# Kernel tuning notes

Hardware: AMD Instinct MI355X
Metric: run time of the kernel (lower is better)

Reference implementation:

```python
import jax, jax.numpy as jnp
import numpy as np

N = 50000
E = 800000
NODE_IN = 128
HID = 256
OUT = 256
EDGE_DIM = 16
HEADS = 4
CH = HID // HEADS  # 64
NEG_SLOPE = 0.2


def _init_linear(key, fan_in, fan_out):
    k1, k2 = jax.random.split(key)
    bound = 1.0 / np.sqrt(fan_in)
    W = jax.random.uniform(k1, (fan_in, fan_out), jnp.float32, -bound, bound)
    b = jax.random.uniform(k2, (fan_out,), jnp.float32, -bound, bound)
    return W, b


def setup_inputs() -> dict:
    key = jax.random.key(0)
    ks = jax.random.split(key, 12)
    node_feats = jax.random.normal(ks[0], (N, NODE_IN), jnp.float32)
    edge_index = jax.random.randint(ks[1], (2, E), 0, N, jnp.int64)
    edge_attr = jax.random.normal(ks[2], (E, EDGE_DIM), jnp.float32)

    Wnp, bnp = _init_linear(ks[3], NODE_IN, HID)           # node_proj
    Wep, bep = _init_linear(ks[4], EDGE_DIM, HID)          # edge_proj
    # GATConv 1: in = 2*HID, out per head = CH
    Wg1, _ = _init_linear(ks[5], 2 * HID, HEADS * CH)
    as1 = jax.random.normal(ks[6], (HEADS, CH), jnp.float32) * 0.1
    ad1 = jax.random.normal(ks[7], (HEADS, CH), jnp.float32) * 0.1
    bg1 = jnp.zeros((HEADS * CH,), jnp.float32)
    # GATConv 2: in = HID, out per head = OUT//HEADS
    Wg2, _ = _init_linear(ks[8], HID, HEADS * (OUT // HEADS))
    as2 = jax.random.normal(ks[9], (HEADS, OUT // HEADS), jnp.float32) * 0.1
    ad2 = jax.random.normal(ks[10], (HEADS, OUT // HEADS), jnp.float32) * 0.1
    bg2 = jnp.zeros((OUT,), jnp.float32)
    Wo, bo = _init_linear(ks[11], OUT, OUT)                # out_proj
    return {
        "node_feats": node_feats, "edge_attr": edge_attr,
        "Wnp": Wnp, "bnp": bnp, "Wep": Wep, "bep": bep,
        "Wg1": Wg1, "as1": as1, "ad1": ad1, "bg1": bg1,
        "Wg2": Wg2, "as2": as2, "ad2": ad2, "bg2": bg2,
        "Wo": Wo, "bo": bo,
        "edge_index": edge_index,
    }


def scatter_mean(src, index, num_nodes):
    # mean of edge features grouped by target node; empty groups -> 0 (count clamped to 1)
    s = jax.ops.segment_sum(src, index, num_segments=num_nodes)
    cnt = jax.ops.segment_sum(jnp.ones((src.shape[0],), src.dtype), index, num_segments=num_nodes)
    return s / jnp.maximum(cnt, 1.0)[:, None]


def gat_conv(x, src, dst, W, att_src, att_dst, bias, num_nodes, heads, ch):
    # PyG GATConv with add_self_loops=True (loops appended by caller via src/dst),
    # concat=True, negative_slope=0.2.
    xh = (x @ W).reshape(num_nodes, heads, ch)             # [N,H,C]
    a_src = jnp.sum(xh * att_src, axis=-1)                 # [N,H]
    a_dst = jnp.sum(xh * att_dst, axis=-1)                 # [N,H]
    logits = jax.nn.leaky_relu(a_src[src] + a_dst[dst], NEG_SLOPE)  # [E,H]
    # segment softmax over incoming edges of each destination node
    m = jax.ops.segment_max(logits, dst, num_segments=num_nodes)    # [N,H]
    ex = jnp.exp(logits - m[dst])
    denom = jax.ops.segment_sum(ex, dst, num_segments=num_nodes)    # [N,H]
    alpha = ex / denom[dst]                                          # [E,H]
    msg = xh[src] * alpha[:, :, None]                                # [E,H,C]
    out = jax.ops.segment_sum(msg, dst, num_segments=num_nodes)      # [N,H,C]
    return out.reshape(num_nodes, heads * ch) + bias


def reference(node_feats, edge_attr, Wnp, bnp, Wep, bep,
              Wg1, as1, ad1, bg1, Wg2, as2, ad2, bg2, Wo, bo, edge_index):
    n = node_feats.shape[0]
    x = node_feats @ Wnp + bnp                                       # [N,HID]
    # EdgeAggregator: mean of edge_attr over target nodes, then edge_proj
    nef = scatter_mean(edge_attr, edge_index[1], n)                  # [N,EDGE_DIM]
    nef = nef @ Wep + bep                                            # [N,HID]
    x = jnp.concatenate([x, nef], axis=-1)                           # [N,2*HID]
    # add self loops once (same augmented edge set for both GAT layers)
    loops = jnp.arange(n, dtype=edge_index.dtype)
    src = jnp.concatenate([edge_index[0], loops])
    dst = jnp.concatenate([edge_index[1], loops])
    x = jax.nn.elu(gat_conv(x, src, dst, Wg1, as1, ad1, bg1, n, HEADS, CH))
    # dropout is identity in eval mode
    x = jax.nn.elu(gat_conv(x, src, dst, Wg2, as2, ad2, bg2, n, HEADS, OUT // HEADS))
    return x @ Wo + bo
```

## Files before the change

kernel.cpp:

```cpp
#include <hip/hip_runtime.h>
#include <hip/hip_bf16.h>


#define HEADS 4

typedef __attribute__((ext_vector_type(8))) short bf16x8;
typedef __attribute__((ext_vector_type(4))) float f32x4;
typedef __attribute__((ext_vector_type(4))) unsigned short u16x4;

__device__ __forceinline__ unsigned short f2b(float v) {
    __hip_bfloat16 b = __float2bfloat16(v);
    return __builtin_bit_cast(unsigned short, b);
}
__device__ __forceinline__ float b2f(unsigned short u) {
    __hip_bfloat16 b = __builtin_bit_cast(__hip_bfloat16, u);
    return __bfloat162float(b);
}
__device__ __forceinline__ void split_hilo(float v, unsigned short& h, unsigned short& l) {
    h = f2b(v);
    l = f2b(v - b2f(h));
}
__device__ __forceinline__ unsigned short f2h(float v) {
    _Float16 h = (_Float16)v;
    return __builtin_bit_cast(unsigned short, h);
}
__device__ __forceinline__ float h2f(unsigned short u) {
    return (float)__builtin_bit_cast(_Float16, u);
}
__device__ __forceinline__ void gl2lds16(const unsigned short* g, unsigned short* l) {
    __builtin_amdgcn_global_load_lds(
        (const __attribute__((address_space(1))) unsigned int*)g,
        (__attribute__((address_space(3))) unsigned int*)l,
        16, 0, 0);
}


__global__ __launch_bounds__(256) void count_kernel(
    const int* __restrict__ dst, int* __restrict__ cnt, int E)
{
    int e = blockIdx.x * 256 + threadIdx.x;
    if (e < E) atomicAdd(&cnt[dst[e]], 1);
}

__global__ __launch_bounds__(256) void scan1_kernel(
    const int* __restrict__ cnt, int* __restrict__ chunk_sum, int N)
{
    __shared__ int sd[256];
    int t = threadIdx.x;
    int n = blockIdx.x * 256 + t;
    sd[t] = (n < N) ? (cnt[n] + 1) : 0;
    __syncthreads();
    for (int o = 128; o > 0; o >>= 1) {
        if (t < o) sd[t] += sd[t + o];
        __syncthreads();
    }
    if (t == 0) chunk_sum[blockIdx.x] = sd[0];
}

__global__ __launch_bounds__(256) void scan2_kernel(
    const int* __restrict__ chunk_sum, int* __restrict__ chunk_off, int nchunk)
{
    __shared__ int sd[256];
    __shared__ int carry;
    int t = threadIdx.x;
    if (t == 0) carry = 0;
    __syncthreads();
    for (int b = 0; b < nchunk; b += 256) {
        int i = b + t;
        int v = (i < nchunk) ? chunk_sum[i] : 0;
        sd[t] = v;
        __syncthreads();
        for (int o = 1; o < 256; o <<= 1) {
            int x = (t >= o) ? sd[t - o] : 0;
            __syncthreads();
            sd[t] += x;
            __syncthreads();
        }
        if (i < nchunk) chunk_off[i] = carry + sd[t] - v;
        __syncthreads();
        if (t == 0) carry += sd[255];
        __syncthreads();
    }
}

__global__ __launch_bounds__(256) void scan3_kernel(
    const int* __restrict__ cnt, const int* __restrict__ chunk_off,
    int* __restrict__ rowptr, int* __restrict__ fillptr,
    int* __restrict__ col, int* __restrict__ eid, int N)
{
    __shared__ int sd[256];
    int t = threadIdx.x;
    int n = blockIdx.x * 256 + t;
    int v = (n < N) ? (cnt[n] + 1) : 0;
    sd[t] = v;
    __syncthreads();
    for (int o = 1; o < 256; o <<= 1) {
        int x = (t >= o) ? sd[t - o] : 0;
        __syncthreads();
        sd[t] += x;
        __syncthreads();
    }
    if (n < N) {
        int incl = sd[t];
        int r = chunk_off[blockIdx.x] + incl - v;
        rowptr[n] = r;
        col[r] = n;
        eid[r] = -1;
        fillptr[n] = r + 1;
        if (n == N - 1) rowptr[N] = chunk_off[blockIdx.x] + incl;
    }
}

__global__ __launch_bounds__(256) void fill_kernel(
    const int* __restrict__ src, const int* __restrict__ dst,
    int* __restrict__ fillptr, int* __restrict__ col, int* __restrict__ eid, int E)
{
    int e = blockIdx.x * 256 + threadIdx.x;
    if (e >= E) return;
    int d = dst[e];
    int p = atomicAdd(&fillptr[d], 1);
    col[p] = src[e];
    eid[p] = e;
}

__global__ __launch_bounds__(256) void nef_csr_kernel(
    const float* __restrict__ ea, const int* __restrict__ rowptr,
    const int* __restrict__ eid,
    unsigned short* __restrict__ AH, unsigned short* __restrict__ AL, int N)
{
    int n = blockIdx.x * 4 + (threadIdx.x >> 6);
    if (n >= N) return;
    int t = threadIdx.x & 63;
    int f = t & 15, g = t >> 4;
    int base = rowptr[n], end = rowptr[n + 1];
    int deg = end - base - 1;
    float acc = 0.0f;
    for (int j = base + 1 + g; j < end; j += 4) {
        int e = eid[j];
        acc += ea[(size_t)e * 16 + f];
    }
    acc += __shfl_down(acc, 32, 64);
    acc += __shfl_down(acc, 16, 64);
    if (t < 16) {
        float v = acc / fmaxf((float)deg, 1.0f);
        unsigned short h, l;
        split_hilo(v, h, l);
        AH[(size_t)n * 160 + 128 + t] = h;
        AL[(size_t)n * 160 + 128 + t] = l;
    } else if (t < 32) {
        AH[(size_t)n * 160 + 128 + t] = 0;
        AL[(size_t)n * 160 + 128 + t] = 0;
    }
}

__global__ __launch_bounds__(256) void conv_hilo_strided_kernel(
    const float* __restrict__ X,
    unsigned short* __restrict__ H, unsigned short* __restrict__ L, int total)
{
    int base = (blockIdx.x * 256 + threadIdx.x) * 2;
    if (base >= total) return;
    #pragma unroll
    for (int i = 0; i < 2; i++) {
        int e = base + i;
        int row = e >> 7, c = e & 127;
        unsigned short h, l;
        split_hilo(X[e], h, l);
        H[(size_t)row * 160 + c] = h;
        L[(size_t)row * 160 + c] = l;
    }
}

__global__ __launch_bounds__(256) void compose_w1_kernel(
    const float* __restrict__ Wnp, const float* __restrict__ Wep,
    const float* __restrict__ bnp, const float* __restrict__ bep,
    const float* __restrict__ Wg1,
    float* __restrict__ Wc, float* __restrict__ c1)
{
    int idx = blockIdx.x * 256 + threadIdx.x;
    if (idx >= 145 * 256) return;
    int i = idx >> 8, j = idx & 255;
    float s = 0.0f;
    if (i < 128) {
        for (int k = 0; k < 256; k++) s += Wnp[i * 256 + k] * Wg1[(size_t)k * 256 + j];
        Wc[i * 256 + j] = s;
    } else if (i < 144) {
        int ii = i - 128;
        for (int k = 0; k < 256; k++) s += Wep[ii * 256 + k] * Wg1[(size_t)(256 + k) * 256 + j];
        Wc[i * 256 + j] = s;
    } else {
        for (int k = 0; k < 256; k++)
            s += bnp[k] * Wg1[(size_t)k * 256 + j] + bep[k] * Wg1[(size_t)(256 + k) * 256 + j];
        c1[j] = s;
    }
}

__device__ __forceinline__ void pack_one(
    const float* __restrict__ W, int K, int KP, int idx,
    unsigned short* __restrict__ Ph, unsigned short* __restrict__ Pl)
{
    int tile = idx >> 9, w = idx & 511, lane = w >> 3, j = w & 7;
    int nk = KP >> 5;
    int ctile = tile / nk, t = tile % nk;
    int k = t * 32 + ((lane >> 4) << 3) + j;
    int n = (ctile << 4) + (lane & 15);
    float v = (k < K) ? W[(size_t)k * 256 + n] : 0.0f;
    unsigned short h, l;
    split_hilo(v, h, l);
    Ph[idx] = h;
    Pl[idx] = l;
}

__global__ __launch_bounds__(256) void pack3_w_kernel(
    const float* __restrict__ Wc,  unsigned short* __restrict__ PcH,  unsigned short* __restrict__ PcL,
    const float* __restrict__ Wg2, unsigned short* __restrict__ Pg2H, unsigned short* __restrict__ Pg2L,
    const float* __restrict__ Wo,  unsigned short* __restrict__ PoH,  unsigned short* __restrict__ PoL)
{
    const int S0 = 160 * 256;
    const int S1 = S0 + 256 * 256;
    const int S2 = S1 + 256 * 256;
    int idx = blockIdx.x * 256 + threadIdx.x;
    if (idx < S0) {
        pack_one(Wc, 144, 160, idx, PcH, PcL);
    } else if (idx < S1) {
        pack_one(Wg2, 256, 256, idx - S0, Pg2H, Pg2L);
    } else if (idx < S2) {
        pack_one(Wo, 256, 256, idx - S1, PoH, PoL);
    }
}

template <int KSTEPS, int OMODE, bool FUSE_ATT>
__global__ __launch_bounds__(256, 5) void mfma_gemm_kernel(
    const unsigned short* __restrict__ Ah, const unsigned short* __restrict__ Al,
    int lda,
    const unsigned short* __restrict__ Ph, const unsigned short* __restrict__ Pl,
    const float* __restrict__ bias,
    float* __restrict__ Cf,
    unsigned short* __restrict__ Ch, unsigned short* __restrict__ Cl,
    int ldc, int col_off, int Nrows,
    const float* __restrict__ att_src, const float* __restrict__ att_dst,
    float* __restrict__ a_srcO, float* __restrict__ a_dstO)
{
    __shared__ unsigned short ldsB[2][2][8][512];
    int tid = threadIdx.x;
    int wave = tid >> 6, lane = tid & 63;
    int quad = lane >> 4, m16 = lane & 15;
    int rowblk = blockIdx.x, colhalf = blockIdx.y;
    int ctile0 = colhalf * 8;

    int row = rowblk * 64 + wave * 16 + m16;
    bool rowok = row < Nrows;
    const unsigned short* arh = Ah + (size_t)row * lda;
    const unsigned short* arl = Al + (size_t)row * lda;

    auto stage = [&](int t, int buf) {
        #pragma unroll
        for (int q = 0; q < 2; q++) {
            int c = wave * 2 + q;
            size_t gb = ((size_t)((ctile0 + c) * KSTEPS + t)) * 512 + lane * 8;
            gl2lds16(Ph + gb, &ldsB[buf][0][c][0]);
            gl2lds16(Pl + gb, &ldsB[buf][1][c][0]);
        }
    };
    auto loadA = [&](int t, bf16x8& h, bf16x8& l) {
        int k = t * 32 + quad * 8;
        h = (bf16x8){};
        l = (bf16x8){};
        if (rowok) {
            h = *(const bf16x8*)(arh + k);
            l = *(const bf16x8*)(arl + k);
        }
    };

    f32x4 acc[8] = {};
    bf16x8 ah2[2], al2[2];
    loadA(0, ah2[0], al2[0]);
    stage(0, 0);
    __syncthreads();

    #pragma unroll
    for (int t = 0; t < KSTEPS; t++) {
        const int buf = t & 1;
        if (t + 1 < KSTEPS) {
            stage(t + 1, buf ^ 1);
            loadA(t + 1, ah2[(t + 1) & 1], al2[(t + 1) & 1]);
        }
        #pragma unroll
        for (int c = 0; c < 8; c++) {
            bf16x8 b_h = *(const bf16x8*)&ldsB[buf][0][c][lane * 8];
            bf16x8 b_l = *(const bf16x8*)&ldsB[buf][1][c][lane * 8];
            acc[c] = __builtin_amdgcn_mfma_f32_16x16x32_bf16(ah2[buf], b_h, acc[c], 0, 0, 0);
            acc[c] = __builtin_amdgcn_mfma_f32_16x16x32_bf16(al2[buf], b_h, acc[c], 0, 0, 0);
            acc[c] = __builtin_amdgcn_mfma_f32_16x16x32_bf16(ah2[buf], b_l, acc[c], 0, 0, 0);
        }
        if (t + 1 < KSTEPS) __syncthreads();
    }

    #pragma unroll
    for (int c = 0; c < 8; c++) {
        int ocol = (ctile0 + c) * 16 + m16;
        float bv = bias ? bias[ocol] : 0.0f;
        #pragma unroll
        for (int r = 0; r < 4; r++) {
            int orow = rowblk * 64 + wave * 16 + quad * 4 + r;
            if (orow >= Nrows) continue;
            float v = acc[c][r] + bv;
            size_t oidx = (size_t)orow * ldc + col_off + ocol;
            if (OMODE == 1) {
                unsigned short h, l;
                split_hilo(v, h, l);
                Ch[oidx] = h;
                Cl[oidx] = l;
            } else if (OMODE == 2) {
                Ch[oidx] = f2h(v);
            } else {
                Cf[oidx] = v;
            }
        }
    }

    if (FUSE_ATT) {
        float ps[4][2] = {}, pd[4][2] = {};
        #pragma unroll
        for (int c = 0; c < 8; c++) {
            int ocol = (ctile0 + c) * 16 + m16;
            float bv = bias ? bias[ocol] : 0.0f;
            float asv = att_src[ocol];
            float adv = att_dst[ocol];
            int hl = c >> 2;
            #pragma unroll
            for (int r = 0; r < 4; r++) {
                float v = acc[c][r] + bv;
                ps[r][hl] += v * asv;
                pd[r][hl] += v * adv;
            }
        }
        #pragma unroll
        for (int r = 0; r < 4; r++) {
            #pragma unroll
            for (int hl = 0; hl < 2; hl++) {
                float s = ps[r][hl], d = pd[r][hl];
                #pragma unroll
                for (int o = 8; o > 0; o >>= 1) {
                    s += __shfl_down(s, o, 64);
                    d += __shfl_down(d, o, 64);
                }
                if (m16 == 0) {
                    int orow = rowblk * 64 + wave * 16 + quad * 4 + r;
                    if (orow < Nrows) {
                        int gh = colhalf * 2 + hl;
                        a_srcO[orow * 4 + gh] = s;
                        a_dstO[orow * 4 + gh] = d;
                    }
                }
            }
        }
    }
}

__global__ __launch_bounds__(256) void edge_w_kernel(
    const int* __restrict__ rowptr, const int* __restrict__ col,
    const float* __restrict__ a_src, const float* __restrict__ a_dst,
    float* __restrict__ wq, float* __restrict__ den, int N)
{
    int n = blockIdx.x * 4 + (threadIdx.x >> 6);
    if (n >= N) return;
    int lane = threadIdx.x & 63;
    int base = rowptr[n], end = rowptr[n + 1];
    float4 ad = *(const float4*)&a_dst[n * 4];
    float4 ds = {0.0f, 0.0f, 0.0f, 0.0f};
    for (int j = base + lane; j < end; j += 64) {
        int s = col[j];
        float4 as4 = *(const float4*)&a_src[s * 4];
        float l0 = as4.x + ad.x, l1 = as4.y + ad.y;
        float l2 = as4.z + ad.z, l3 = as4.w + ad.w;
        l0 = fmaxf(l0, 0.2f * l0);
        l1 = fmaxf(l1, 0.2f * l1);
        l2 = fmaxf(l2, 0.2f * l2);
        l3 = fmaxf(l3, 0.2f * l3);
        float4 wv = {__expf(l0), __expf(l1), __expf(l2), __expf(l3)};
        *(float4*)&wq[(size_t)j * 4] = wv;
        ds.x += wv.x; ds.y += wv.y; ds.z += wv.z; ds.w += wv.w;
    }
    #pragma unroll
    for (int o = 32; o > 0; o >>= 1) {
        ds.x += __shfl_down(ds.x, o, 64);
        ds.y += __shfl_down(ds.y, o, 64);
        ds.z += __shfl_down(ds.z, o, 64);
        ds.w += __shfl_down(ds.w, o, 64);
    }
    if (lane == 0) *(float4*)&den[n * 4] = ds;
}

__global__ __launch_bounds__(256) void gat_agg_csr_kernel(
    const unsigned short* __restrict__ xh,
    const int* __restrict__ rowptr, const int* __restrict__ col,
    const float* __restrict__ wq, const float* __restrict__ den,
    const float* __restrict__ bias,
    unsigned short* __restrict__ outH, unsigned short* __restrict__ outL, int N)
{
    int t = threadIdx.x;
    int n = blockIdx.x * 4 + (t >> 6);
    if (n >= N) return;
    int c = t & 63;
    int h = c >> 4;
    int base = rowptr[n], end = rowptr[n + 1];
    int e1 = end - 1;
    float inv = 1.0f / den[n * 4 + h];
    const unsigned short* xcol = xh + (c << 2);

    float4 acc = {0.0f, 0.0f, 0.0f, 0.0f};
    for (int j = base; j < end; j += 4) {
        int j1 = j + 1 < e1 ? j + 1 : e1;
        int j2 = j + 2 < e1 ? j + 2 : e1;
        int j3 = j + 3 < e1 ? j + 3 : e1;
        int s0 = col[j], s1 = col[j1], s2 = col[j2], s3 = col[j3];
        float w0 = wq[(size_t)j * 4 + h];
        float w1 = (j + 1 < end) ? wq[(size_t)j1 * 4 + h] : 0.0f;
        float w2 = (j + 2 < end) ? wq[(size_t)j2 * 4 + h] : 0.0f;
        float w3 = (j + 3 < end) ? wq[(size_t)j3 * 4 + h] : 0.0f;
        u16x4 x0 = *(const u16x4*)(xcol + (size_t)s0 * 256);
        u16x4 x1 = *(const u16x4*)(xcol + (size_t)s1 * 256);
        u16x4 x2 = *(const u16x4*)(xcol + (size_t)s2 * 256);
        u16x4 x3 = *(const u16x4*)(xcol + (size_t)s3 * 256);
        acc.x += w0 * h2f(x0[0]) + w1 * h2f(x1[0]) + w2 * h2f(x2[0]) + w3 * h2f(x3[0]);
        acc.y += w0 * h2f(x0[1]) + w1 * h2f(x1[1]) + w2 * h2f(x2[1]) + w3 * h2f(x3[1]);
        acc.z += w0 * h2f(x0[2]) + w1 * h2f(x1[2]) + w2 * h2f(x2[2]) + w3 * h2f(x3[2]);
        acc.w += w0 * h2f(x0[3]) + w1 * h2f(x1[3]) + w2 * h2f(x2[3]) + w3 * h2f(x3[3]);
    }

    float4 bv = *(const float4*)(bias + (c << 2));
    float o0 = acc.x * inv + bv.x;
    float o1 = acc.y * inv + bv.y;
    float o2 = acc.z * inv + bv.z;
    float o3 = acc.w * inv + bv.w;
    o0 = (o0 > 0.0f) ? o0 : (__expf(o0) - 1.0f);
    o1 = (o1 > 0.0f) ? o1 : (__expf(o1) - 1.0f);
    o2 = (o2 > 0.0f) ? o2 : (__expf(o2) - 1.0f);
    o3 = (o3 > 0.0f) ? o3 : (__expf(o3) - 1.0f);
    u16x4 H, L;
    split_hilo(o0, ((unsigned short*)&H)[0], ((unsigned short*)&L)[0]);
    split_hilo(o1, ((unsigned short*)&H)[1], ((unsigned short*)&L)[1]);
    split_hilo(o2, ((unsigned short*)&H)[2], ((unsigned short*)&L)[2]);
    split_hilo(o3, ((unsigned short*)&H)[3], ((unsigned short*)&L)[3]);
    *(u16x4*)(&outH[(size_t)n * 256 + (c << 2)]) = H;
    *(u16x4*)(&outL[(size_t)n * 256 + (c << 2)]) = L;
}


extern "C" void kernel_launch(void* const* d_in, const int* in_sizes, int n_in,
                              void* d_out, int out_size, void* d_ws, size_t ws_size,
                              hipStream_t stream)
{
    const float* node_feats = (const float*)d_in[0];
    const float* edge_attr  = (const float*)d_in[1];
    const float* Wnp = (const float*)d_in[2];
    const float* bnp = (const float*)d_in[3];
    const float* Wep = (const float*)d_in[4];
    const float* bep = (const float*)d_in[5];
    const float* Wg1 = (const float*)d_in[6];
    const float* as1 = (const float*)d_in[7];
    const float* ad1 = (const float*)d_in[8];
    const float* bg1 = (const float*)d_in[9];
    const float* Wg2 = (const float*)d_in[10];
    const float* as2 = (const float*)d_in[11];
    const float* ad2 = (const float*)d_in[12];
    const float* bg2 = (const float*)d_in[13];
    const float* Wo  = (const float*)d_in[14];
    const float* bo  = (const float*)d_in[15];
    const int*   ei  = (const int*)d_in[16];

    const int N = in_sizes[0] / 128;
    const int E = in_sizes[16] / 2;
    const int* src = ei;
    const int* dst = ei + E;
    const int nchunk = (N + 255) / 256;
    const int EN = E + N;

    typedef unsigned short u16;

    char* base = (char*)d_ws;
    size_t off = 0;
    auto alloc = [&](size_t bytes) -> char* {
        char* p = base + off;
        off += (bytes + 255) & ~(size_t)255;
        return p;
    };
    u16* xhh = (u16*)alloc((size_t)N * 256 * 2);
    u16* R2  = (u16*)alloc((size_t)N * 512 * 2);
    u16* R3  = (u16*)alloc((size_t)N * 512 * 2);
    float* a_src = (float*)alloc((size_t)N * 4 * 4);
    float* a_dst = (float*)alloc((size_t)N * 4 * 4);
    float* wq    = (float*)alloc((size_t)EN * 4 * 4);
    float* den   = (float*)alloc((size_t)N * 4 * 4);
    float* Wc    = (float*)alloc(144 * 256 * 4);
    float* c1    = (float*)alloc(256 * 4);
    u16* PcH  = (u16*)alloc(160 * 256 * 2);
    u16* PcL  = (u16*)alloc(160 * 256 * 2);
    u16* Pg2H = (u16*)alloc(256 * 256 * 2);
    u16* Pg2L = (u16*)alloc(256 * 256 * 2);
    u16* PoH  = (u16*)alloc(256 * 256 * 2);
    u16* PoL  = (u16*)alloc(256 * 256 * 2);
    int* cnt       = (int*)alloc((size_t)N * 4);
    int* rowptr    = (int*)alloc((size_t)(N + 1) * 4);
    int* fillptr   = (int*)alloc((size_t)N * 4);
    int* chunk_sum = (int*)alloc((size_t)nchunk * 4);
    int* chunk_off = (int*)alloc((size_t)nchunk * 4);
    int* colv      = (int*)alloc((size_t)EN * 4);
    int* eid       = (int*)alloc((size_t)EN * 4);

    u16* AcatH = R2;
    u16* AcatL = R3;
    u16* x3H = R2;
    u16* x3L = R2 + (size_t)N * 256;
    u16* x4H = R3;
    u16* x4L = R3 + (size_t)N * 256;

    float* out = (float*)d_out;
    dim3 ggrid((N + 63) / 64, 2);

    hipMemsetAsync(cnt, 0, (size_t)N * sizeof(int), stream);
    count_kernel<<<(E + 255) / 256, 256, 0, stream>>>(dst, cnt, E);
    scan1_kernel<<<nchunk, 256, 0, stream>>>(cnt, chunk_sum, N);
    scan2_kernel<<<1, 256, 0, stream>>>(chunk_sum, chunk_off, nchunk);
    scan3_kernel<<<nchunk, 256, 0, stream>>>(cnt, chunk_off, rowptr, fillptr, colv, eid, N);
    fill_kernel<<<(E + 255) / 256, 256, 0, stream>>>(src, dst, fillptr, colv, eid, E);

    nef_csr_kernel<<<(N + 3) / 4, 256, 0, stream>>>(edge_attr, rowptr, eid, AcatH, AcatL, N);
    conv_hilo_strided_kernel<<<((N * 128) / 2 + 255) / 256, 256, 0, stream>>>(
        node_feats, AcatH, AcatL, N * 128);
    compose_w1_kernel<<<145, 256, 0, stream>>>(Wnp, Wep, bnp, bep, Wg1, Wc, c1);
    {
        const int total = 160 * 256 + 256 * 256 + 256 * 256;
        pack3_w_kernel<<<(total + 255) / 256, 256, 0, stream>>>(
            Wc, PcH, PcL, Wg2, Pg2H, Pg2L, Wo, PoH, PoL);
    }

    mfma_gemm_kernel<5, 2, true><<<ggrid, 256, 0, stream>>>(
        AcatH, AcatL, 160, PcH, PcL, c1, nullptr, xhh, nullptr, 256, 0, N,
        as1, ad1, a_src, a_dst);
    edge_w_kernel<<<(N + 3) / 4, 256, 0, stream>>>(
        rowptr, colv, a_src, a_dst, wq, den, N);
    gat_agg_csr_kernel<<<(N + 3) / 4, 256, 0, stream>>>(
        xhh, rowptr, colv, wq, den, bg1, x3H, x3L, N);

    mfma_gemm_kernel<8, 2, true><<<ggrid, 256, 0, stream>>>(
        x3H, x3L, 256, Pg2H, Pg2L, nullptr, nullptr, xhh, nullptr, 256, 0, N,
        as2, ad2, a_src, a_dst);
    edge_w_kernel<<<(N + 3) / 4, 256, 0, stream>>>(
        rowptr, colv, a_src, a_dst, wq, den, N);
    gat_agg_csr_kernel<<<(N + 3) / 4, 256, 0, stream>>>(
        xhh, rowptr, colv, wq, den, bg2, x4H, x4L, N);

    mfma_gemm_kernel<8, 0, false><<<ggrid, 256, 0, stream>>>(
        x4H, x4L, 256, PoH, PoL, bo, out, nullptr, nullptr, 256, 0, N,
        nullptr, nullptr, nullptr, nullptr);
}
```

Before: 571.5 us.

## Fuse edge softmax weights into aggregation and store GEMM inputs as fp16

```diff
diff --git a/kernel.cpp b/kernel.cpp
--- a/kernel.cpp
+++ b/kernel.cpp
@@ -7,6 +7,7 @@
 typedef __attribute__((ext_vector_type(8))) short bf16x8;
 typedef __attribute__((ext_vector_type(4))) float f32x4;
 typedef __attribute__((ext_vector_type(4))) unsigned short u16x4;
+typedef __attribute__((ext_vector_type(8))) unsigned short u16x8;
 
 __device__ __forceinline__ unsigned short f2b(float v) {
     __hip_bfloat16 b = __float2bfloat16(v);
@@ -126,7 +127,7 @@
 __global__ __launch_bounds__(256) void nef_csr_kernel(
     const float* __restrict__ ea, const int* __restrict__ rowptr,
     const int* __restrict__ eid,
-    unsigned short* __restrict__ AH, unsigned short* __restrict__ AL, int N)
+    unsigned short* __restrict__ AF, int N)
 {
     int n = blockIdx.x * 4 + (threadIdx.x >> 6);
     if (n >= N) return;
@@ -143,19 +144,14 @@
     acc += __shfl_down(acc, 16, 64);
     if (t < 16) {
         float v = acc / fmaxf((float)deg, 1.0f);
-        unsigned short h, l;
-        split_hilo(v, h, l);
-        AH[(size_t)n * 160 + 128 + t] = h;
-        AL[(size_t)n * 160 + 128 + t] = l;
+        AF[(size_t)n * 160 + 128 + t] = f2h(v);
     } else if (t < 32) {
-        AH[(size_t)n * 160 + 128 + t] = 0;
-        AL[(size_t)n * 160 + 128 + t] = 0;
-    }
-}
-
-__global__ __launch_bounds__(256) void conv_hilo_strided_kernel(
-    const float* __restrict__ X,
-    unsigned short* __restrict__ H, unsigned short* __restrict__ L, int total)
+        AF[(size_t)n * 160 + 128 + t] = 0;
+    }
+}
+
+__global__ __launch_bounds__(256) void conv_f16_strided_kernel(
+    const float* __restrict__ X, unsigned short* __restrict__ AF, int total)
 {
     int base = (blockIdx.x * 256 + threadIdx.x) * 2;
     if (base >= total) return;
@@ -163,10 +159,7 @@
     for (int i = 0; i < 2; i++) {
         int e = base + i;
         int row = e >> 7, c = e & 127;
-        unsigned short h, l;
-        split_hilo(X[e], h, l);
-        H[(size_t)row * 160 + c] = h;
-        L[(size_t)row * 160 + c] = l;
+        AF[(size_t)row * 160 + c] = f2h(X[e]);
     }
 }
 
@@ -228,7 +221,7 @@
     }
 }
 
-template <int KSTEPS, int OMODE, bool FUSE_ATT>
+template <int KSTEPS, int AMODE, int OMODE, bool FUSE_ATT>
 __global__ __launch_bounds__(256, 5) void mfma_gemm_kernel(
     const unsigned short* __restrict__ Ah, const unsigned short* __restrict__ Al,
     int lda,
@@ -250,7 +243,7 @@
     int row = rowblk * 64 + wave * 16 + m16;
     bool rowok = row < Nrows;
     const unsigned short* arh = Ah + (size_t)row * lda;
-    const unsigned short* arl = Al + (size_t)row * lda;
+    const unsigned short* arl = (AMODE == 0) ? (Al + (size_t)row * lda) : nullptr;
 
     auto stage = [&](int t, int buf) {
         #pragma unroll
@@ -266,8 +259,20 @@
         h = (bf16x8){};
         l = (bf16x8){};
         if (rowok) {
-            h = *(const bf16x8*)(arh + k);
-            l = *(const bf16x8*)(arl + k);
+            if (AMODE == 0) {
+                h = *(const bf16x8*)(arh + k);
+                l = *(const bf16x8*)(arl + k);
+            } else {
+                u16x8 v = *(const u16x8*)(arh + k);
+                #pragma unroll
+                for (int i = 0; i < 8; i++) {
+                    float f = h2f(v[i]);
+                    unsigned short hh, ll;
+                    split_hilo(f, hh, ll);
+                    ((unsigned short*)&h)[i] = hh;
+                    ((unsigned short*)&l)[i] = ll;
+                }
+            }
         }
     };
 
@@ -357,77 +362,108 @@
     }
 }
 
-__global__ __launch_bounds__(256) void edge_w_kernel(
-    const int* __restrict__ rowptr, const int* __restrict__ col,
-    const float* __restrict__ a_src, const float* __restrict__ a_dst,
-    float* __restrict__ wq, float* __restrict__ den, int N)
-{
-    int n = blockIdx.x * 4 + (threadIdx.x >> 6);
-    if (n >= N) return;
-    int lane = threadIdx.x & 63;
-    int base = rowptr[n], end = rowptr[n + 1];
-    float4 ad = *(const float4*)&a_dst[n * 4];
-    float4 ds = {0.0f, 0.0f, 0.0f, 0.0f};
-    for (int j = base + lane; j < end; j += 64) {
-        int s = col[j];
-        float4 as4 = *(const float4*)&a_src[s * 4];
-        float l0 = as4.x + ad.x, l1 = as4.y + ad.y;
-        float l2 = as4.z + ad.z, l3 = as4.w + ad.w;
-        l0 = fmaxf(l0, 0.2f * l0);
-        l1 = fmaxf(l1, 0.2f * l1);
-        l2 = fmaxf(l2, 0.2f * l2);
-        l3 = fmaxf(l3, 0.2f * l3);
-        float4 wv = {__expf(l0), __expf(l1), __expf(l2), __expf(l3)};
-        *(float4*)&wq[(size_t)j * 4] = wv;
-        ds.x += wv.x; ds.y += wv.y; ds.z += wv.z; ds.w += wv.w;
-    }
-    #pragma unroll
-    for (int o = 32; o > 0; o >>= 1) {
-        ds.x += __shfl_down(ds.x, o, 64);
-        ds.y += __shfl_down(ds.y, o, 64);
-        ds.z += __shfl_down(ds.z, o, 64);
-        ds.w += __shfl_down(ds.w, o, 64);
-    }
-    if (lane == 0) *(float4*)&den[n * 4] = ds;
-}
-
+template <bool OUTF16>
 __global__ __launch_bounds__(256) void gat_agg_csr_kernel(
     const unsigned short* __restrict__ xh,
     const int* __restrict__ rowptr, const int* __restrict__ col,
-    const float* __restrict__ wq, const float* __restrict__ den,
+    const float* __restrict__ a_src, const float* __restrict__ a_dst,
     const float* __restrict__ bias,
-    unsigned short* __restrict__ outH, unsigned short* __restrict__ outL, int N)
-{
+    unsigned short* __restrict__ outA, unsigned short* __restrict__ outB, int N)
+{
+    __shared__ float wlds[4][128][HEADS];
     int t = threadIdx.x;
-    int n = blockIdx.x * 4 + (t >> 6);
+    int wv = t >> 6;
+    int n = blockIdx.x * 4 + wv;
     if (n >= N) return;
     int c = t & 63;
     int h = c >> 4;
     int base = rowptr[n], end = rowptr[n + 1];
+    int deg = end - base;
     int e1 = end - 1;
-    float inv = 1.0f / den[n * 4 + h];
+    float4 ad = *(const float4*)&a_dst[n * 4];
+    float adh = (h == 0) ? ad.x : (h == 1) ? ad.y : (h == 2) ? ad.z : ad.w;
     const unsigned short* xcol = xh + (c << 2);
 
     float4 acc = {0.0f, 0.0f, 0.0f, 0.0f};
-    for (int j = base; j < end; j += 4) {
-        int j1 = j + 1 < e1 ? j + 1 : e1;
-        int j2 = j + 2 < e1 ? j + 2 : e1;
-        int j3 = j + 3 < e1 ? j + 3 : e1;
-        int s0 = col[j], s1 = col[j1], s2 = col[j2], s3 = col[j3];
-        float w0 = wq[(size_t)j * 4 + h];
-        float w1 = (j + 1 < end) ? wq[(size_t)j1 * 4 + h] : 0.0f;
-        float w2 = (j + 2 < end) ? wq[(size_t)j2 * 4 + h] : 0.0f;
-        float w3 = (j + 3 < end) ? wq[(size_t)j3 * 4 + h] : 0.0f;
-        u16x4 x0 = *(const u16x4*)(xcol + (size_t)s0 * 256);
-        u16x4 x1 = *(const u16x4*)(xcol + (size_t)s1 * 256);
-        u16x4 x2 = *(const u16x4*)(xcol + (size_t)s2 * 256);
-        u16x4 x3 = *(const u16x4*)(xcol + (size_t)s3 * 256);
-        acc.x += w0 * h2f(x0[0]) + w1 * h2f(x1[0]) + w2 * h2f(x2[0]) + w3 * h2f(x3[0]);
-        acc.y += w0 * h2f(x0[1]) + w1 * h2f(x1[1]) + w2 * h2f(x2[1]) + w3 * h2f(x3[1]);
-        acc.z += w0 * h2f(x0[2]) + w1 * h2f(x1[2]) + w2 * h2f(x2[2]) + w3 * h2f(x3[2]);
-        acc.w += w0 * h2f(x0[3]) + w1 * h2f(x1[3]) + w2 * h2f(x2[3]) + w3 * h2f(x3[3]);
-    }
-
+    float den = 0.0f;
+
+    if (deg <= 128) {
+        float4 ds = {0.0f, 0.0f, 0.0f, 0.0f};
+        for (int j = base + c; j < end; j += 64) {
+            int s = col[j];
+            float4 as4 = *(const float4*)&a_src[s * 4];
+            float l0 = as4.x + ad.x, l1 = as4.y + ad.y;
+            float l2 = as4.z + ad.z, l3 = as4.w + ad.w;
+            l0 = fmaxf(l0, 0.2f * l0);
+            l1 = fmaxf(l1, 0.2f * l1);
+            l2 = fmaxf(l2, 0.2f * l2);
+            l3 = fmaxf(l3, 0.2f * l3);
+            float4 wv4 = {__expf(l0), __expf(l1), __expf(l2), __expf(l3)};
+            *(float4*)&wlds[wv][j - base][0] = wv4;
+            ds.x += wv4.x; ds.y += wv4.y; ds.z += wv4.z; ds.w += wv4.w;
+        }
+        #pragma unroll
+        for (int o = 32; o > 0; o >>= 1) {
+            ds.x += __shfl_down(ds.x, o, 64);
+            ds.y += __shfl_down(ds.y, o, 64);
+            ds.z += __shfl_down(ds.z, o, 64);
+            ds.w += __shfl_down(ds.w, o, 64);
+        }
+        float d0 = __shfl(ds.x, 0, 64);
+        float d1 = __shfl(ds.y, 0, 64);
+        float d2 = __shfl(ds.z, 0, 64);
+        float d3 = __shfl(ds.w, 0, 64);
+        den = (h == 0) ? d0 : (h == 1) ? d1 : (h == 2) ? d2 : d3;
+
+        for (int j = base; j < end; j += 4) {
+            int j1 = j + 1 < e1 ? j + 1 : e1;
+            int j2 = j + 2 < e1 ? j + 2 : e1;
+            int j3 = j + 3 < e1 ? j + 3 : e1;
+            int s0 = col[j], s1 = col[j1], s2 = col[j2], s3 = col[j3];
+            float w0 = wlds[wv][j - base][h];
+            float w1 = (j + 1 < end) ? wlds[wv][j1 - base][h] : 0.0f;
+            float w2 = (j + 2 < end) ? wlds[wv][j2 - base][h] : 0.0f;
+            float w3 = (j + 3 < end) ? wlds[wv][j3 - base][h] : 0.0f;
+            u16x4 x0 = *(const u16x4*)(xcol + (size_t)s0 * 256);
+            u16x4 x1 = *(const u16x4*)(xcol + (size_t)s1 * 256);
+            u16x4 x2 = *(const u16x4*)(xcol + (size_t)s2 * 256);
+            u16x4 x3 = *(const u16x4*)(xcol + (size_t)s3 * 256);
+            acc.x += w0 * h2f(x0[0]) + w1 * h2f(x1[0]) + w2 * h2f(x2[0]) + w3 * h2f(x3[0]);
+            acc.y += w0 * h2f(x0[1]) + w1 * h2f(x1[1]) + w2 * h2f(x2[1]) + w3 * h2f(x3[1]);
+            acc.z += w0 * h2f(x0[2]) + w1 * h2f(x1[2]) + w2 * h2f(x2[2]) + w3 * h2f(x3[2]);
+            acc.w += w0 * h2f(x0[3]) + w1 * h2f(x1[3]) + w2 * h2f(x2[3]) + w3 * h2f(x3[3]);
+        }
+    } else {
+        for (int j = base; j < end; j += 4) {
+            int j1 = j + 1 < e1 ? j + 1 : e1;
+            int j2 = j + 2 < e1 ? j + 2 : e1;
+            int j3 = j + 3 < e1 ? j + 3 : e1;
+            int s0 = col[j], s1 = col[j1], s2 = col[j2], s3 = col[j3];
+            float l0 = a_src[s0 * 4 + h] + adh;
+            float l1 = a_src[s1 * 4 + h] + adh;
+            float l2 = a_src[s2 * 4 + h] + adh;
+            float l3 = a_src[s3 * 4 + h] + adh;
+            l0 = fmaxf(l0, 0.2f * l0);
+            l1 = fmaxf(l1, 0.2f * l1);
+            l2 = fmaxf(l2, 0.2f * l2);
+            l3 = fmaxf(l3, 0.2f * l3);
+            float w0 = __expf(l0);
+            float w1 = (j + 1 < end) ? __expf(l1) : 0.0f;
+            float w2 = (j + 2 < end) ? __expf(l2) : 0.0f;
+            float w3 = (j + 3 < end) ? __expf(l3) : 0.0f;
+            u16x4 x0 = *(const u16x4*)(xcol + (size_t)s0 * 256);
+            u16x4 x1 = *(const u16x4*)(xcol + (size_t)s1 * 256);
+            u16x4 x2 = *(const u16x4*)(xcol + (size_t)s2 * 256);
+            u16x4 x3 = *(const u16x4*)(xcol + (size_t)s3 * 256);
+            den += (w0 + w1) + (w2 + w3);
+            acc.x += w0 * h2f(x0[0]) + w1 * h2f(x1[0]) + w2 * h2f(x2[0]) + w3 * h2f(x3[0]);
+            acc.y += w0 * h2f(x0[1]) + w1 * h2f(x1[1]) + w2 * h2f(x2[1]) + w3 * h2f(x3[1]);
+            acc.z += w0 * h2f(x0[2]) + w1 * h2f(x1[2]) + w2 * h2f(x2[2]) + w3 * h2f(x3[2]);
+            acc.w += w0 * h2f(x0[3]) + w1 * h2f(x1[3]) + w2 * h2f(x2[3]) + w3 * h2f(x3[3]);
+        }
+    }
+
+    float inv = 1.0f / den;
     float4 bv = *(const float4*)(bias + (c << 2));
     float o0 = acc.x * inv + bv.x;
     float o1 = acc.y * inv + bv.y;
@@ -437,13 +473,19 @@
     o1 = (o1 > 0.0f) ? o1 : (__expf(o1) - 1.0f);
     o2 = (o2 > 0.0f) ? o2 : (__expf(o2) - 1.0f);
     o3 = (o3 > 0.0f) ? o3 : (__expf(o3) - 1.0f);
-    u16x4 H, L;
-    split_hilo(o0, ((unsigned short*)&H)[0], ((unsigned short*)&L)[0]);
-    split_hilo(o1, ((unsigned short*)&H)[1], ((unsigned short*)&L)[1]);
-    split_hilo(o2, ((unsigned short*)&H)[2], ((unsigned short*)&L)[2]);
-    split_hilo(o3, ((unsigned short*)&H)[3], ((unsigned short*)&L)[3]);
-    *(u16x4*)(&outH[(size_t)n * 256 + (c << 2)]) = H;
-    *(u16x4*)(&outL[(size_t)n * 256 + (c << 2)]) = L;
+    if (OUTF16) {
+        u16x4 H;
+        H[0] = f2h(o0); H[1] = f2h(o1); H[2] = f2h(o2); H[3] = f2h(o3);
+        *(u16x4*)(&outA[(size_t)n * 256 + (c << 2)]) = H;
+    } else {
+        u16x4 H, L;
+        split_hilo(o0, ((unsigned short*)&H)[0], ((unsigned short*)&L)[0]);
+        split_hilo(o1, ((unsigned short*)&H)[1], ((unsigned short*)&L)[1]);
+        split_hilo(o2, ((unsigned short*)&H)[2], ((unsigned short*)&L)[2]);
+        split_hilo(o3, ((unsigned short*)&H)[3], ((unsigned short*)&L)[3]);
+        *(u16x4*)(&outA[(size_t)n * 256 + (c << 2)]) = H;
+        *(u16x4*)(&outB[(size_t)n * 256 + (c << 2)]) = L;
+    }
 }
 
 
@@ -490,8 +532,6 @@
     u16* R3  = (u16*)alloc((size_t)N * 512 * 2);
     float* a_src = (float*)alloc((size_t)N * 4 * 4);
     float* a_dst = (float*)alloc((size_t)N * 4 * 4);
-    float* wq    = (float*)alloc((size_t)EN * 4 * 4);
-    float* den   = (float*)alloc((size_t)N * 4 * 4);
     float* Wc    = (float*)alloc(144 * 256 * 4);
     float* c1    = (float*)alloc(256 * 4);
     u16* PcH  = (u16*)alloc(160 * 256 * 2);
@@ -508,10 +548,8 @@
     int* colv      = (int*)alloc((size_t)EN * 4);
     int* eid       = (int*)alloc((size_t)EN * 4);
 
-    u16* AcatH = R2;
-    u16* AcatL = R3;
-    u16* x3H = R2;
-    u16* x3L = R2 + (size_t)N * 256;
+    u16* AcatF = R2;
+    u16* x3F   = R2;
     u16* x4H = R3;
     u16* x4L = R3 + (size_t)N * 256;
 
@@ -525,9 +563,9 @@
     scan3_kernel<<<nchunk, 256, 0, stream>>>(cnt, chunk_off, rowptr, fillptr, colv, eid, N);
     fill_kernel<<<(E + 255) / 256, 256, 0, stream>>>(src, dst, fillptr, colv, eid, E);
 
-    nef_csr_kernel<<<(N + 3) / 4, 256, 0, stream>>>(edge_attr, rowptr, eid, AcatH, AcatL, N);
-    conv_hilo_strided_kernel<<<((N * 128) / 2 + 255) / 256, 256, 0, stream>>>(
-        node_feats, AcatH, AcatL, N * 128);
+    nef_csr_kernel<<<(N + 3) / 4, 256, 0, stream>>>(edge_attr, rowptr, eid, AcatF, N);
+    conv_f16_strided_kernel<<<((N * 128) / 2 + 255) / 256, 256, 0, stream>>>(
+        node_feats, AcatF, N * 128);
     compose_w1_kernel<<<145, 256, 0, stream>>>(Wnp, Wep, bnp, bep, Wg1, Wc, c1);
     {
         const int total = 160 * 256 + 256 * 256 + 256 * 256;
@@ -535,23 +573,19 @@
             Wc, PcH, PcL, Wg2, Pg2H, Pg2L, Wo, PoH, PoL);
     }
 
-    mfma_gemm_kernel<5, 2, true><<<ggrid, 256, 0, stream>>>(
-        AcatH, AcatL, 160, PcH, PcL, c1, nullptr, xhh, nullptr, 256, 0, N,
+    mfma_gemm_kernel<5, 1, 2, true><<<ggrid, 256, 0, stream>>>(
+        AcatF, nullptr, 160, PcH, PcL, c1, nullptr, xhh, nullptr, 256, 0, N,
         as1, ad1, a_src, a_dst);
-    edge_w_kernel<<<(N + 3) / 4, 256, 0, stream>>>(
-        rowptr, colv, a_src, a_dst, wq, den, N);
-    gat_agg_csr_kernel<<<(N + 3) / 4, 256, 0, stream>>>(
-        xhh, rowptr, colv, wq, den, bg1, x3H, x3L, N);
-
-    mfma_gemm_kernel<8, 2, true><<<ggrid, 256, 0, stream>>>(
-        x3H, x3L, 256, Pg2H, Pg2L, nullptr, nullptr, xhh, nullptr, 256, 0, N,
+    gat_agg_csr_kernel<true><<<(N + 3) / 4, 256, 0, stream>>>(
+        xhh, rowptr, colv, a_src, a_dst, bg1, x3F, nullptr, N);
+
+    mfma_gemm_kernel<8, 1, 2, true><<<ggrid, 256, 0, stream>>>(
+        x3F, nullptr, 256, Pg2H, Pg2L, nullptr, nullptr, xhh, nullptr, 256, 0, N,
         as2, ad2, a_src, a_dst);
-    edge_w_kernel<<<(N + 3) / 4, 256, 0, stream>>>(
-        rowptr, colv, a_src, a_dst, wq, den, N);
-    gat_agg_csr_kernel<<<(N + 3) / 4, 256, 0, stream>>>(
-        xhh, rowptr, colv, wq, den, bg2, x4H, x4L, N);
-
-    mfma_gemm_kernel<8, 0, false><<<ggrid, 256, 0, stream>>>(
+    gat_agg_csr_kernel<false><<<(N + 3) / 4, 256, 0, stream>>>(
+        xhh, rowptr, colv, a_src, a_dst, bg2, x4H, x4L, N);
+
+    mfma_gemm_kernel<8, 0, 0, false><<<ggrid, 256, 0, stream>>>(
         x4H, x4L, 256, PoH, PoL, bo, out, nullptr, nullptr, 256, 0, N,
         nullptr, nullptr, nullptr, nullptr);
 }
```

New measurement: 540.4 us. 5.4% less time.
